# Optimization experiments

Hardware: AMD Instinct MI355X
Metric: run time of the kernel (lower is better)

The kernel has to match this reference:

```python
import jax, jax.numpy as jnp
import numpy as np

R, E, NU, NI = 5, 50000, 20000, 20000
NF, DN, DR, DO = 4, 16, 64, 64   # num_factor, node/msg dim (64//NF), review dim (msg_units*NF), out_units
TAU = 0.5


def _l2norm(x):
    n = jnp.maximum(jnp.linalg.norm(x, axis=-1, keepdims=True), 1e-12)
    return x / n


def setup_inputs() -> dict:
    key = jax.random.key(0)
    ks = jax.random.split(key, 18)
    s = 0.1  # keep exp() arguments in a sane range / xavier-ish weight scale
    return {
        "user_h": jax.random.normal(ks[0], (NF, R, NU, DN), jnp.float32),
        "item_h": jax.random.normal(ks[1], (NF, R, NI, DN), jnp.float32),
        "user_hsum": jax.random.normal(ks[2], (R, NU, NF, DN), jnp.float32) * s,
        "item_hsum": jax.random.normal(ks[3], (R, NI, NF, DN), jnp.float32) * s,
        "review_feat": jax.random.normal(ks[4], (R, E, NF, DR), jnp.float32) * s,
        "prototypes": jax.random.normal(ks[5], (NF, DR), jnp.float32) * s,
        "eta": jax.random.normal(ks[6], (R, E), jnp.float32),
        "node_w_fwd": jax.random.normal(ks[7], (R, DN, DN), jnp.float32) * s,
        "review_w_fwd": jax.random.normal(ks[8], (R, DN, DR), jnp.float32) * s,
        "node_w_rev": jax.random.normal(ks[9], (R, DN, DN), jnp.float32) * s,
        "review_w_rev": jax.random.normal(ks[10], (R, DN, DR), jnp.float32) * s,
        "ufc_w": jax.random.normal(ks[11], (DO, DN), jnp.float32) * s,
        "ufc_b": jnp.zeros((DO,), jnp.float32),
        "ifc_w": jax.random.normal(ks[12], (DO, DN), jnp.float32) * s,
        "ifc_b": jnp.zeros((DO,), jnp.float32),
        "edge_src": jax.random.randint(ks[13], (R, E), 0, NU),
        "edge_dst": jax.random.randint(ks[14], (R, E), 0, NI),
        "k": 1,
    }


def reference(user_h, item_h, user_hsum, item_hsum, review_feat, prototypes,
              eta, node_w_fwd, review_w_fwd, node_w_rev, review_w_rev,
              ufc_w, ufc_b, ifc_w, ifc_b, edge_src, edge_dst, k):
    rI = jnp.arange(R)[:, None]                       # [R,1] rating index for gathers
    uh, ih = user_h[k], item_h[k]                     # [R,N,DN]
    # contrastive similarity on factor k (L2-normalized node feats)
    row_f = _l2norm(uh[rI, edge_src])                 # [R,E,DN]
    col_f = _l2norm(ih[rI, edge_dst])
    sim_k = jnp.sum(row_f * col_f, -1) / TAU          # [R,E]
    row_all = user_hsum[rI, edge_src]                 # [R,E,NF,DN]
    col_all = item_hsum[rI, edge_dst]
    sim_all = jnp.sum(row_all * col_all, -1) / TAU    # [R,E,NF]
    exp_sim = jnp.exp(sim_k) / jnp.sum(jnp.exp(sim_all), -1)
    # prototype (anchor) similarity of review features
    rf_k = review_feat[:, :, k, :]                    # [R,E,DR]
    anchor_k = jnp.einsum('red,d->re', rf_k, prototypes[k]) / TAU
    anchor_all = jnp.einsum('refd,fd->ref', review_feat, prototypes) / TAU
    exp_anchor = jnp.exp(anchor_k) / jnp.sum(jnp.exp(anchor_all), -1)
    g = jax.nn.sigmoid(eta)                           # eta[rating][:E]
    # identical for 'rating' and 'rev-rating' etypes (all dots commute under row/col swap)
    blended = g * exp_anchor + (1.0 - g) * exp_sim    # [R,E]
    flat = blended.reshape(-1)
    src_flat = edge_src.reshape(-1)
    dst_flat = edge_dst.reshape(-1)
    # fwd and rev etypes each contribute an identical scatter; (x + x) / 2 == x
    norm_user = jax.ops.segment_sum(flat, src_flat, num_segments=NU)
    norm_item = jax.ops.segment_sum(flat, dst_flat, num_segments=NI)
    n_ij = jnp.sqrt(norm_user[edge_src] * norm_item[edge_dst])  # [R,E]
    w = blended / n_ij                                # edge weight, same for both directions
    int_dist = w.reshape(R * E, 1)                    # concat of rev-etype weights in rating order
    # GCMCGraphConv per etype: (node_w(h_src)[row] + review_w(rf)) * w, scatter-sum to dst
    hu = jnp.einsum('rnd,rod->rno', uh, node_w_fwd)   # Linear: x @ W.T, per rating
    hi = jnp.einsum('rnd,rod->rno', ih, node_w_rev)
    rfw = jnp.einsum('red,rod->reo', rf_k, review_w_fwd)
    rfr = jnp.einsum('red,rod->reo', rf_k, review_w_rev)
    m_fwd = (hu[rI, edge_src] + rfw) * w[..., None]   # [R,E,DN] user->item messages
    m_rev = (hi[rI, edge_dst] + rfr) * w[..., None]   # item->user messages
    item_msg = jax.ops.segment_sum(m_fwd.reshape(-1, DN), dst_flat, num_segments=NI)
    user_msg = jax.ops.segment_sum(m_rev.reshape(-1, DN), src_flat, num_segments=NU)
    ufeat = jax.nn.leaky_relu(user_msg, 0.1) @ ufc_w.T + ufc_b
    ifeat = jax.nn.leaky_relu(item_msg, 0.1) @ ifc_w.T + ifc_b
    return ufeat, ifeat, int_dist
```

## Files before the change

kernel.cpp:

```cpp
#include <hip/hip_runtime.h>
#include <math.h>

constexpr int R  = 5;
constexpr int E  = 50000;
constexpr int NU = 20000;
constexpr int NI = 20000;
constexpr int NF = 4;
constexpr int DN = 16;
constexpr int DR = 64;
constexpr int DO = 64;
constexpr float TAU = 0.5f;

__global__ __launch_bounds__(256) void pass1_kernel(
    const float* __restrict__ user_h,
    const float* __restrict__ item_h,
    const float* __restrict__ user_hsum,
    const float* __restrict__ item_hsum,
    const float* __restrict__ review_feat,
    const float* __restrict__ prototypes,
    const float* __restrict__ eta,
    const int*   __restrict__ edge_src,
    const int*   __restrict__ edge_dst,
    const int*   __restrict__ kptr,
    float* __restrict__ blended_out,
    float* __restrict__ norm_user,
    float* __restrict__ norm_item)
{
    const int lane = threadIdx.x & 63;
    const int wid  = threadIdx.x >> 6;
    const long long idx = (long long)blockIdx.x * (blockDim.x >> 6) + wid;
    if (idx >= (long long)R * E) return;
    const int r = (int)(idx / E);
    const int e = (int)(idx - (long long)r * E);
    const int k = *kptr;
    const long long re = (long long)r * E + e;

    const int src = edge_src[re];
    const int dst = edge_dst[re];

    float na = 0.f, nb = 0.f, ab = 0.f;
    if (lane < DN) {
        const float* up = user_h + (((long long)k * R + r) * NU + src) * DN;
        const float* ip = item_h + (((long long)k * R + r) * NI + dst) * DN;
        float a = up[lane];
        float b = ip[lane];
        na = a * a; nb = b * b; ab = a * b;
    }
#pragma unroll
    for (int m = 1; m < 16; m <<= 1) {
        na += __shfl_xor(na, m, 64);
        nb += __shfl_xor(nb, m, 64);
        ab += __shfl_xor(ab, m, 64);
    }
    na = __shfl(na, 0, 64);
    nb = __shfl(nb, 0, 64);
    ab = __shfl(ab, 0, 64);
    const float sim_k = ab / (fmaxf(sqrtf(na), 1e-12f) * fmaxf(sqrtf(nb), 1e-12f)) / TAU;

    const float* rs = user_hsum + ((long long)r * NU + src) * (NF * DN);
    const float* cs = item_hsum + ((long long)r * NI + dst) * (NF * DN);
    float p = rs[lane] * cs[lane];
#pragma unroll
    for (int m = 1; m < 16; m <<= 1) p += __shfl_xor(p, m, 64);
    float es = __expf(p / TAU);
    float denom_sim = es;
    denom_sim += __shfl_xor(denom_sim, 16, 64);
    denom_sim += __shfl_xor(denom_sim, 32, 64);

    const float4* rf4 = (const float4*)(review_feat + re * (long long)(NF * DR));
    const float4* pr4 = (const float4*)prototypes;
    float4 rv = rf4[lane];
    float4 pv = pr4[lane];
    float q = rv.x * pv.x + rv.y * pv.y + rv.z * pv.z + rv.w * pv.w;
#pragma unroll
    for (int m = 1; m < 16; m <<= 1) q += __shfl_xor(q, m, 64);
    float ea = __expf(q / TAU);
    float denom_anc = ea;
    denom_anc += __shfl_xor(denom_anc, 16, 64);
    denom_anc += __shfl_xor(denom_anc, 32, 64);
    float ea_k = __shfl(ea, k * 16, 64);

    const float exp_anchor = ea_k / denom_anc;
    const float exp_sim    = __expf(sim_k) / denom_sim;
    const float g = 1.0f / (1.0f + __expf(-eta[re]));
    const float blended = g * exp_anchor + (1.0f - g) * exp_sim;

    if (lane == 0) {
        blended_out[re] = blended;
        atomicAdd(&norm_user[src], blended);
        atomicAdd(&norm_item[dst], blended);
    }
}

__global__ __launch_bounds__(256) void nodexf_kernel(
    const float* __restrict__ user_h,
    const float* __restrict__ item_h,
    const float* __restrict__ node_w_fwd,
    const float* __restrict__ node_w_rev,
    const int*   __restrict__ kptr,
    float* __restrict__ hu_t,
    float* __restrict__ hi_t)
{
    const int r    = blockIdx.y;
    const int side = blockIdx.z;
    const int n0   = blockIdx.x * 64;
    const int k    = *kptr;
    const int N    = side ? NI : NU;
    const float* h    = side ? item_h : user_h;
    const float* wsrc = side ? node_w_rev : node_w_fwd;
    float* out        = side ? hi_t : hu_t;

    __shared__ __align__(16) float lds_h[64 * 16];
    __shared__ float lds_w[16 * 17];

    const int t = threadIdx.x;
    {
        const int o = t >> 4, d = t & 15;
        lds_w[o * 17 + d] = wsrc[((long long)r * DN + o) * DN + d];
    }
    {
        const int row = t >> 2, c = t & 3;
        if (n0 + row < N) {
            const float4 v = *(const float4*)(h + (((long long)k * R + r) * N + n0 + row) * DN + c * 4);
            *(float4*)&lds_h[t * 4] = v;
        }
    }
    __syncthreads();

    const int o = t & 15;
#pragma unroll
    for (int p = 0; p < 4; ++p) {
        const int nl = p * 16 + (t >> 4);
        const int n = n0 + nl;
        if (n < N) {
            float acc = 0.f;
#pragma unroll
            for (int d = 0; d < DN; ++d)
                acc += lds_h[nl * 16 + d] * lds_w[o * 17 + d];
            out[((long long)r * N + n) * DN + o] = acc;
        }
    }
}

__global__ __launch_bounds__(256) void pass2b_kernel(
    const float* __restrict__ hu_t,
    const float* __restrict__ hi_t,
    const float* __restrict__ review_feat,
    const float* __restrict__ review_w_fwd,
    const float* __restrict__ review_w_rev,
    const int*   __restrict__ edge_src,
    const int*   __restrict__ edge_dst,
    const int*   __restrict__ kptr,
    const float* __restrict__ blended,
    const float* __restrict__ norm_user,
    const float* __restrict__ norm_item,
    float* __restrict__ user_msg,
    float* __restrict__ item_msg,
    float* __restrict__ int_dist)
{
    constexpr int EPB = 128, TILE = 16, WPAD = 68;
    const int r  = blockIdx.y;
    const int e0 = blockIdx.x * EPB;
    const int k  = *kptr;
    const int t  = threadIdx.x;

    __shared__ __align__(16) float wf[16 * WPAD];
    __shared__ __align__(16) float wr[16 * WPAD];
    __shared__ __align__(16) float rf[16 * WPAD];

    for (int i = t; i < 16 * 64; i += 256) {
        const int o = i >> 6, d = i & 63;
        wf[o * WPAD + d] = review_w_fwd[((long long)r * DN + o) * DR + d];
        wr[o * WPAD + d] = review_w_rev[((long long)r * DN + o) * DR + d];
    }
    __syncthreads();

    const int el = t >> 4;
    const int o  = t & 15;

    for (int tile = 0; tile < EPB / TILE; ++tile) {
        const int ee = e0 + tile * TILE + el;
        if (ee < E) {
            const float4 v = *(const float4*)(review_feat +
                (((long long)r * E + ee) * NF + k) * DR + o * 4);
            *(float4*)&rf[el * WPAD + o * 4] = v;
        }
        __syncthreads();
        if (ee < E) {
            const int re = r * E + ee;
            float accf = 0.f, accr = 0.f;
#pragma unroll
            for (int c = 0; c < 16; ++c) {
                const float4 a  = *(const float4*)&rf[el * WPAD + c * 4];
                const float4 bf = *(const float4*)&wf[o * WPAD + c * 4];
                const float4 br = *(const float4*)&wr[o * WPAD + c * 4];
                accf += a.x * bf.x + a.y * bf.y + a.z * bf.z + a.w * bf.w;
                accr += a.x * br.x + a.y * br.y + a.z * br.z + a.w * br.w;
            }
            const int src = edge_src[re];
            const int dst = edge_dst[re];
            accf += hu_t[((long long)r * NU + src) * DN + o];
            accr += hi_t[((long long)r * NI + dst) * DN + o];
            const float w = blended[re] * rsqrtf(norm_user[src] * norm_item[dst]);
            if (o == 0) int_dist[re] = w;
            atomicAdd(&item_msg[(long long)dst * DN + o], accf * w);
            atomicAdd(&user_msg[(long long)src * DN + o], accr * w);
        }
        __syncthreads();
    }
}

__global__ __launch_bounds__(256) void pass3_kernel(
    const float* __restrict__ user_msg,
    const float* __restrict__ item_msg,
    const float* __restrict__ ufc_w,
    const float* __restrict__ ufc_b,
    const float* __restrict__ ifc_w,
    const float* __restrict__ ifc_b,
    float* __restrict__ ufeat,
    float* __restrict__ ifeat)
{
    const long long t = (long long)blockIdx.x * blockDim.x + threadIdx.x;
    const long long nu_total = (long long)NU * DO;
    const long long total = nu_total + (long long)NI * DO;
    if (t >= total) return;
    const bool is_item = (t >= nu_total);
    const long long tt = is_item ? (t - nu_total) : t;
    const int j = (int)(tt & 63);
    const long long n = tt >> 6;

    const float* msg  = (is_item ? item_msg : user_msg) + n * DN;
    const float* wrow = (is_item ? ifc_w : ufc_w) + (long long)j * DN;
    float acc = (is_item ? ifc_b : ufc_b)[j];
#pragma unroll
    for (int d = 0; d < DN; ++d) {
        float x = msg[d];
        x = (x > 0.f) ? x : 0.1f * x;
        acc += x * wrow[d];
    }
    (is_item ? ifeat : ufeat)[tt] = acc;
}

extern "C" void kernel_launch(void* const* d_in, const int* in_sizes, int n_in,
                              void* d_out, int out_size, void* d_ws, size_t ws_size,
                              hipStream_t stream) {
    const float* user_h       = (const float*)d_in[0];
    const float* item_h       = (const float*)d_in[1];
    const float* user_hsum    = (const float*)d_in[2];
    const float* item_hsum    = (const float*)d_in[3];
    const float* review_feat  = (const float*)d_in[4];
    const float* prototypes   = (const float*)d_in[5];
    const float* eta          = (const float*)d_in[6];
    const float* node_w_fwd   = (const float*)d_in[7];
    const float* review_w_fwd = (const float*)d_in[8];
    const float* node_w_rev   = (const float*)d_in[9];
    const float* review_w_rev = (const float*)d_in[10];
    const float* ufc_w        = (const float*)d_in[11];
    const float* ufc_b        = (const float*)d_in[12];
    const float* ifc_w        = (const float*)d_in[13];
    const float* ifc_b        = (const float*)d_in[14];
    const int*   edge_src     = (const int*)d_in[15];
    const int*   edge_dst     = (const int*)d_in[16];
    const int*   kptr         = (const int*)d_in[17];

    float* ws = (float*)d_ws;
    float* norm_user = ws;
    float* norm_item = norm_user + NU;
    float* user_msg  = norm_item + NI;
    float* item_msg  = user_msg + (long long)NU * DN;
    float* blended   = item_msg + (long long)NI * DN;
    float* hu_t      = blended + (long long)R * E;
    float* hi_t      = hu_t + (long long)R * NU * DN;

    const size_t zero_bytes = (size_t)(NU + NI + NU * DN + NI * DN) * sizeof(float);
    hipMemsetAsync(d_ws, 0, zero_bytes, stream);

    float* ufeat    = (float*)d_out;
    float* ifeat    = ufeat + (long long)NU * DO;
    float* int_dist = ifeat + (long long)NI * DO;

    {
        dim3 grid((NU + 63) / 64, R, 2);
        nodexf_kernel<<<grid, 256, 0, stream>>>(
            user_h, item_h, node_w_fwd, node_w_rev, kptr, hu_t, hi_t);
    }

    {
        const long long nwaves = (long long)R * E;
        const int blocks = (int)((nwaves + 3) / 4);
        pass1_kernel<<<blocks, 256, 0, stream>>>(
            user_h, item_h, user_hsum, item_hsum, review_feat, prototypes,
            eta, edge_src, edge_dst, kptr, blended, norm_user, norm_item);
    }

    {
        dim3 grid((E + 127) / 128, R);
        pass2b_kernel<<<grid, 256, 0, stream>>>(
            hu_t, hi_t, review_feat, review_w_fwd, review_w_rev,
            edge_src, edge_dst, kptr, blended, norm_user, norm_item,
            user_msg, item_msg, int_dist);
    }

    {
        const long long nthreads = (long long)(NU + NI) * DO;
        const int blocks = (int)((nthreads + 255) / 256);
        pass3_kernel<<<blocks, 256, 0, stream>>>(
            user_msg, item_msg, ufc_w, ufc_b, ifc_w, ifc_b, ufeat, ifeat);
    }
}
```

Before: 561.1 us.

## Pack four edges per wave in pass1 and restructure pass2b thread-to-edge mapping

Pass1 now processes four edges per 64-lane wave, with 16 lanes per edge using float4 loads and shorter shuffle reductions, instead of one edge per wave with mostly idle lanes. Pass2b is restructured so each thread owns one edge and four output channels. It loads the review tile once with a single barrier instead of looping over tiles with repeated syncs, and reads hu/hi with float4 loads. This reduces wasted lanes, shuffle traffic and barriers, but pass1 now assumes E is divisible by 16 and drops its bounds check.

```diff
diff --git a/kernel.cpp b/kernel.cpp
--- a/kernel.cpp
+++ b/kernel.cpp
@@ -10,6 +10,7 @@
 constexpr int DR = 64;
 constexpr int DO = 64;
 constexpr float TAU = 0.5f;
+constexpr float INV_TAU = 2.0f;
 
 __global__ __launch_bounds__(256) void pass1_kernel(
     const float* __restrict__ user_h,
@@ -27,65 +28,64 @@
     float* __restrict__ norm_item)
 {
     const int lane = threadIdx.x & 63;
-    const int wid  = threadIdx.x >> 6;
-    const long long idx = (long long)blockIdx.x * (blockDim.x >> 6) + wid;
-    if (idx >= (long long)R * E) return;
-    const int r = (int)(idx / E);
-    const int e = (int)(idx - (long long)r * E);
-    const int k = *kptr;
-    const long long re = (long long)r * E + e;
+    const int w    = threadIdx.x >> 6;
+    const int r    = blockIdx.y;
+    const int base = (blockIdx.x * 4 + w) * 4;
+    const int k    = *kptr;
+
+    const int e  = lane >> 4;
+    const int le = lane & 15;
+    const int f  = le >> 2;
+    const int j  = le & 3;
+
+    const int ee = base + e;
+    const long long re = (long long)r * E + ee;
 
     const int src = edge_src[re];
     const int dst = edge_dst[re];
 
     float na = 0.f, nb = 0.f, ab = 0.f;
-    if (lane < DN) {
-        const float* up = user_h + (((long long)k * R + r) * NU + src) * DN;
-        const float* ip = item_h + (((long long)k * R + r) * NI + dst) * DN;
-        float a = up[lane];
-        float b = ip[lane];
-        na = a * a; nb = b * b; ab = a * b;
-    }
-#pragma unroll
-    for (int m = 1; m < 16; m <<= 1) {
-        na += __shfl_xor(na, m, 64);
-        nb += __shfl_xor(nb, m, 64);
-        ab += __shfl_xor(ab, m, 64);
-    }
-    na = __shfl(na, 0, 64);
-    nb = __shfl(nb, 0, 64);
-    ab = __shfl(ab, 0, 64);
-    const float sim_k = ab / (fmaxf(sqrtf(na), 1e-12f) * fmaxf(sqrtf(nb), 1e-12f)) / TAU;
-
-    const float* rs = user_hsum + ((long long)r * NU + src) * (NF * DN);
-    const float* cs = item_hsum + ((long long)r * NI + dst) * (NF * DN);
-    float p = rs[lane] * cs[lane];
-#pragma unroll
-    for (int m = 1; m < 16; m <<= 1) p += __shfl_xor(p, m, 64);
-    float es = __expf(p / TAU);
-    float denom_sim = es;
-    denom_sim += __shfl_xor(denom_sim, 16, 64);
-    denom_sim += __shfl_xor(denom_sim, 32, 64);
-
-    const float4* rf4 = (const float4*)(review_feat + re * (long long)(NF * DR));
+    if (f == 0) {
+        const float4 ua = *(const float4*)(user_h + (((long long)k * R + r) * NU + src) * DN + j * 4);
+        const float4 ia = *(const float4*)(item_h + (((long long)k * R + r) * NI + dst) * DN + j * 4);
+        na = ua.x*ua.x + ua.y*ua.y + ua.z*ua.z + ua.w*ua.w;
+        nb = ia.x*ia.x + ia.y*ia.y + ia.z*ia.z + ia.w*ia.w;
+        ab = ua.x*ia.x + ua.y*ia.y + ua.z*ia.z + ua.w*ia.w;
+    }
+    na += __shfl_xor(na, 1, 64); na += __shfl_xor(na, 2, 64);
+    nb += __shfl_xor(nb, 1, 64); nb += __shfl_xor(nb, 2, 64);
+    ab += __shfl_xor(ab, 1, 64); ab += __shfl_xor(ab, 2, 64);
+
+    const float4 rs = *(const float4*)(user_hsum + ((long long)r * NU + src) * (NF * DN) + le * 4);
+    const float4 cs = *(const float4*)(item_hsum + ((long long)r * NI + dst) * (NF * DN) + le * 4);
+    float p = rs.x*cs.x + rs.y*cs.y + rs.z*cs.z + rs.w*cs.w;
+    p += __shfl_xor(p, 1, 64); p += __shfl_xor(p, 2, 64);
+    float denom_sim = __expf(p * INV_TAU);
+    denom_sim += __shfl_xor(denom_sim, 4, 64);
+    denom_sim += __shfl_xor(denom_sim, 8, 64);
+
+    const float4* rf4 = (const float4*)review_feat + re * (NF * DR / 4);
     const float4* pr4 = (const float4*)prototypes;
-    float4 rv = rf4[lane];
-    float4 pv = pr4[lane];
-    float q = rv.x * pv.x + rv.y * pv.y + rv.z * pv.z + rv.w * pv.w;
-#pragma unroll
-    for (int m = 1; m < 16; m <<= 1) q += __shfl_xor(q, m, 64);
-    float ea = __expf(q / TAU);
+    float q = 0.f;
+#pragma unroll
+    for (int c = 0; c < 4; ++c) {
+        const float4 a = rf4[f * 16 + c * 4 + j];
+        const float4 b = pr4[f * 16 + c * 4 + j];
+        q += a.x*b.x + a.y*b.y + a.z*b.z + a.w*b.w;
+    }
+    q += __shfl_xor(q, 1, 64); q += __shfl_xor(q, 2, 64);
+    float ea = __expf(q * INV_TAU);
     float denom_anc = ea;
-    denom_anc += __shfl_xor(denom_anc, 16, 64);
-    denom_anc += __shfl_xor(denom_anc, 32, 64);
-    float ea_k = __shfl(ea, k * 16, 64);
-
-    const float exp_anchor = ea_k / denom_anc;
-    const float exp_sim    = __expf(sim_k) / denom_sim;
-    const float g = 1.0f / (1.0f + __expf(-eta[re]));
-    const float blended = g * exp_anchor + (1.0f - g) * exp_sim;
-
-    if (lane == 0) {
+    denom_anc += __shfl_xor(denom_anc, 4, 64);
+    denom_anc += __shfl_xor(denom_anc, 8, 64);
+    const float ea_k = __shfl(ea, (lane & 48) | (k << 2), 64);
+
+    if (le == 0) {
+        const float sim_k = ab / (fmaxf(sqrtf(na), 1e-12f) * fmaxf(sqrtf(nb), 1e-12f)) * INV_TAU;
+        const float exp_anchor = ea_k / denom_anc;
+        const float exp_sim    = __expf(sim_k) / denom_sim;
+        const float g = 1.0f / (1.0f + __expf(-eta[re]));
+        const float blended = g * exp_anchor + (1.0f - g) * exp_sim;
         blended_out[re] = blended;
         atomicAdd(&norm_user[src], blended);
         atomicAdd(&norm_item[dst], blended);
@@ -158,55 +158,71 @@
     float* __restrict__ item_msg,
     float* __restrict__ int_dist)
 {
-    constexpr int EPB = 128, TILE = 16, WPAD = 68;
-    const int r  = blockIdx.y;
-    const int e0 = blockIdx.x * EPB;
-    const int k  = *kptr;
-    const int t  = threadIdx.x;
-
-    __shared__ __align__(16) float wf[16 * WPAD];
-    __shared__ __align__(16) float wr[16 * WPAD];
-    __shared__ __align__(16) float rf[16 * WPAD];
-
-    for (int i = t; i < 16 * 64; i += 256) {
-        const int o = i >> 6, d = i & 63;
-        wf[o * WPAD + d] = review_w_fwd[((long long)r * DN + o) * DR + d];
-        wr[o * WPAD + d] = review_w_rev[((long long)r * DN + o) * DR + d];
+    constexpr int EPB = 64;
+    constexpr int RSTRIDE = 68;
+    const int r    = blockIdx.y;
+    const int e0   = blockIdx.x * EPB;
+    const int k    = *kptr;
+    const int t    = threadIdx.x;
+    const int lane = t & 63;
+    const int w    = t >> 6;
+
+    __shared__ __align__(16) float wf[DN * DR];
+    __shared__ __align__(16) float wr[DN * DR];
+    __shared__ __align__(16) float rf[EPB * RSTRIDE];
+
+    {
+        const int i = t * 4;
+        *(float4*)&wf[i] = *(const float4*)(review_w_fwd + (long long)r * (DN * DR) + i);
+        *(float4*)&wr[i] = *(const float4*)(review_w_rev + (long long)r * (DN * DR) + i);
+    }
+    {
+        const int row = t >> 2;
+        const int c0  = (t & 3) * 16;
+        const int ee  = e0 + row;
+        if (ee < E) {
+            const float4* s = (const float4*)(review_feat +
+                (((long long)r * E + ee) * NF + k) * DR + c0);
+            float4* d = (float4*)&rf[row * RSTRIDE + c0];
+            d[0] = s[0]; d[1] = s[1]; d[2] = s[2]; d[3] = s[3];
+        }
     }
     __syncthreads();
 
-    const int el = t >> 4;
-    const int o  = t & 15;
-
-    for (int tile = 0; tile < EPB / TILE; ++tile) {
-        const int ee = e0 + tile * TILE + el;
-        if (ee < E) {
-            const float4 v = *(const float4*)(review_feat +
-                (((long long)r * E + ee) * NF + k) * DR + o * 4);
-            *(float4*)&rf[el * WPAD + o * 4] = v;
+    const int ee = e0 + lane;
+    const int ob = w * 4;
+    float accf[4] = {0.f, 0.f, 0.f, 0.f};
+    float accr[4] = {0.f, 0.f, 0.f, 0.f};
+
+    const float* rfrow = &rf[lane * RSTRIDE];
+#pragma unroll 4
+    for (int c = 0; c < 16; ++c) {
+        const float4 a = *(const float4*)&rfrow[c * 4];
+#pragma unroll
+        for (int jj = 0; jj < 4; ++jj) {
+            const float4 bf = *(const float4*)&wf[(ob + jj) * DR + c * 4];
+            const float4 br = *(const float4*)&wr[(ob + jj) * DR + c * 4];
+            accf[jj] += a.x*bf.x + a.y*bf.y + a.z*bf.z + a.w*bf.w;
+            accr[jj] += a.x*br.x + a.y*br.y + a.z*br.z + a.w*br.w;
         }
-        __syncthreads();
-        if (ee < E) {
-            const int re = r * E + ee;
-            float accf = 0.f, accr = 0.f;
-#pragma unroll
-            for (int c = 0; c < 16; ++c) {
-                const float4 a  = *(const float4*)&rf[el * WPAD + c * 4];
-                const float4 bf = *(const float4*)&wf[o * WPAD + c * 4];
-                const float4 br = *(const float4*)&wr[o * WPAD + c * 4];
-                accf += a.x * bf.x + a.y * bf.y + a.z * bf.z + a.w * bf.w;
-                accr += a.x * br.x + a.y * br.y + a.z * br.z + a.w * br.w;
-            }
-            const int src = edge_src[re];
-            const int dst = edge_dst[re];
-            accf += hu_t[((long long)r * NU + src) * DN + o];
-            accr += hi_t[((long long)r * NI + dst) * DN + o];
-            const float w = blended[re] * rsqrtf(norm_user[src] * norm_item[dst]);
-            if (o == 0) int_dist[re] = w;
-            atomicAdd(&item_msg[(long long)dst * DN + o], accf * w);
-            atomicAdd(&user_msg[(long long)src * DN + o], accr * w);
-        }
-        __syncthreads();
+    }
+
+    if (ee < E) {
+        const long long re = (long long)r * E + ee;
+        const int src = edge_src[re];
+        const int dst = edge_dst[re];
+        const float wgt = blended[re] * rsqrtf(norm_user[src] * norm_item[dst]);
+        if (w == 0) int_dist[re] = wgt;
+        const float4 hu = *(const float4*)(hu_t + ((long long)r * NU + src) * DN + ob);
+        const float4 hi = *(const float4*)(hi_t + ((long long)r * NI + dst) * DN + ob);
+        atomicAdd(&item_msg[(long long)dst * DN + ob + 0], (accf[0] + hu.x) * wgt);
+        atomicAdd(&item_msg[(long long)dst * DN + ob + 1], (accf[1] + hu.y) * wgt);
+        atomicAdd(&item_msg[(long long)dst * DN + ob + 2], (accf[2] + hu.z) * wgt);
+        atomicAdd(&item_msg[(long long)dst * DN + ob + 3], (accf[3] + hu.w) * wgt);
+        atomicAdd(&user_msg[(long long)src * DN + ob + 0], (accr[0] + hi.x) * wgt);
+        atomicAdd(&user_msg[(long long)src * DN + ob + 1], (accr[1] + hi.y) * wgt);
+        atomicAdd(&user_msg[(long long)src * DN + ob + 2], (accr[2] + hi.z) * wgt);
+        atomicAdd(&user_msg[(long long)src * DN + ob + 3], (accr[3] + hi.w) * wgt);
     }
 }
 
@@ -286,15 +302,14 @@
     }
 
     {
-        const long long nwaves = (long long)R * E;
-        const int blocks = (int)((nwaves + 3) / 4);
-        pass1_kernel<<<blocks, 256, 0, stream>>>(
+        dim3 grid(E / 16, R);
+        pass1_kernel<<<grid, 256, 0, stream>>>(
             user_h, item_h, user_hsum, item_hsum, review_feat, prototypes,
             eta, edge_src, edge_dst, kptr, blended, norm_user, norm_item);
     }
 
     {
-        dim3 grid((E + 127) / 128, R);
+        dim3 grid((E + 63) / 64, R);
         pass2b_kernel<<<grid, 256, 0, stream>>>(
             hu_t, hi_t, review_feat, review_w_fwd, review_w_rev,
             edge_src, edge_dst, kptr, blended, norm_user, norm_item,
```

Result: slower. 877.8 us (+56.4%).
